# Optimization experiments

Measured on AMD Instinct MI355X. Metric: run time of the kernel, lower is better.

## Reference

```python
import jax, jax.numpy as jnp
import numpy as np

D = 1024        # n_embed
POS = 512       # n_pos_embed
H = 16          # heads
HS = D // H     # head size
DFF = 4 * D     # mlp hidden
EPS = 1e-5


def layernorm(x, g, b, eps=EPS):
    mu = jnp.mean(x, axis=-1, keepdims=True)
    var = jnp.var(x, axis=-1, keepdims=True)
    return (x - mu) * jax.lax.rsqrt(var + eps) * g + b


def setup_inputs() -> dict:
    key = jax.random.key(0)
    ks = jax.random.split(key, 12)
    std = 0.02
    inp = {
        "grid": jax.random.normal(ks[0], (8, 24, 24, D), dtype=jnp.float32),
        "query_pos": jax.random.normal(ks[1], (8, 1024, POS), dtype=jnp.float32),
        "Wq": jax.random.normal(ks[2], (POS, D), dtype=jnp.float32) * std,
        "Wk": jax.random.normal(ks[3], (D, D), dtype=jnp.float32) * std,
        "Wv": jax.random.normal(ks[4], (D, D), dtype=jnp.float32) * std,
        "Wo": jax.random.normal(ks[5], (D, D), dtype=jnp.float32) * std,
        "ln_grid_g": jnp.ones((D,), jnp.float32),
        "ln_grid_b": jnp.zeros((D,), jnp.float32),
        "ln_q_g": jnp.ones((POS,), jnp.float32),
        "ln_q_b": jnp.zeros((POS,), jnp.float32),
        "ln_mlp_g": jnp.ones((D,), jnp.float32),
        "ln_mlp_b": jnp.zeros((D,), jnp.float32),
        "W1": jax.random.normal(ks[6], (D, DFF), dtype=jnp.float32) * std,
        "b1": jnp.zeros((DFF,), jnp.float32),
        "W2": jax.random.normal(ks[7], (DFF, D), dtype=jnp.float32) * std,
        "b2": jnp.zeros((D,), jnp.float32),
    }
    return inp


def reference(grid, query_pos, Wq, Wk, Wv, Wo, ln_grid_g, ln_grid_b,
              ln_q_g, ln_q_b, ln_mlp_g, ln_mlp_b, W1, b1, W2, b2):
    B, N, M, d = grid.shape
    T = N * M
    grid_flat = grid.reshape(B, T, d)
    grid_norm = layernorm(grid_flat, ln_grid_g, ln_grid_b)
    K = jnp.einsum('btd,de->bte', grid_norm, Wk)
    V = jnp.einsum('btd,de->bte', grid_norm, Wv)
    query_norm = layernorm(query_pos, ln_q_g, ln_q_b)
    Q = jnp.einsum('blp,pe->ble', query_norm, Wq)
    L = Q.shape[1]
    # split heads: (B, H, L, HS)
    Qh = Q.reshape(B, L, H, HS).transpose(0, 2, 1, 3)
    Kh = K.reshape(B, T, H, HS).transpose(0, 2, 1, 3)
    Vh = V.reshape(B, T, H, HS).transpose(0, 2, 1, 3)
    scale = 1.0 / np.sqrt(HS).astype(np.float32)
    scores = jnp.einsum('bhld,bhmd->bhlm', Qh, Kh) * scale
    probs = jax.nn.softmax(scores, axis=-1)
    attn = jnp.einsum('bhlm,bhmd->bhld', probs, Vh)
    attn = attn.transpose(0, 2, 1, 3).reshape(B, L, d)
    attn = jnp.einsum('bld,de->ble', attn, Wo)
    x = Q + attn  # Q_proj residual
    x_norm = layernorm(x, ln_mlp_g, ln_mlp_b)
    mlp = jax.nn.gelu(x_norm @ W1 + b1) @ W2 + b2
    return x + mlp
```

## Files before the change

### kernel.cpp

```cpp
#include <hip/hip_runtime.h>

typedef __bf16 bf16x8 __attribute__((ext_vector_type(8)));
typedef float  f32x4  __attribute__((ext_vector_type(4)));
typedef short  s16x8  __attribute__((ext_vector_type(8)));

__device__ __forceinline__ unsigned short f2b(float f) {
  unsigned int u = __float_as_uint(f);
  u += 0x7fffu + ((u >> 16) & 1u);
  return (unsigned short)(u >> 16);
}
__device__ __forceinline__ float b2f(unsigned short h) {
  return __uint_as_float(((unsigned int)h) << 16);
}

__device__ __forceinline__ void gload_lds16(const unsigned short* g, unsigned short* l) {
  __builtin_amdgcn_global_load_lds((const __attribute__((address_space(1))) void*)g,
                                   (__attribute__((address_space(3))) void*)l, 16, 0, 0);
}

__device__ __forceinline__ void bar() {
  __builtin_amdgcn_sched_barrier(0);
  asm volatile("" ::: "memory");
  __builtin_amdgcn_s_barrier();
  asm volatile("" ::: "memory");
  __builtin_amdgcn_sched_barrier(0);
}

#define WAIT_LGKM0 do { asm volatile("s_waitcnt lgkmcnt(0)" ::: "memory"); \
                        __builtin_amdgcn_sched_barrier(0); } while (0)

__global__ __launch_bounds__(256) void transpose_w(const float* __restrict__ in,
                                                   unsigned short* __restrict__ out,
                                                   int R, int C) {
  __shared__ float t[32][33];
  int c0 = blockIdx.x * 32, r0 = blockIdx.y * 32;
  int tx = threadIdx.x & 31, ty = threadIdx.x >> 5;
  for (int i = ty; i < 32; i += 8)
    t[i][tx] = in[(size_t)(r0 + i) * C + (c0 + tx)];
  __syncthreads();
  for (int i = ty; i < 32; i += 8)
    out[(size_t)(c0 + i) * R + (r0 + tx)] = f2b(t[tx][i]);
}

__global__ __launch_bounds__(256) void ln_kernel(const float* __restrict__ in,
                                                 const float* __restrict__ g,
                                                 const float* __restrict__ b,
                                                 unsigned short* __restrict__ out,
                                                 int cols) {
  int row = blockIdx.x;
  const float* x = in + (size_t)row * cols;
  float s = 0.f, s2 = 0.f;
  for (int c = threadIdx.x * 4; c < cols; c += 1024) {
    float4 v = *(const float4*)(x + c);
    s  += v.x + v.y + v.z + v.w;
    s2 += v.x * v.x + v.y * v.y + v.z * v.z + v.w * v.w;
  }
#pragma unroll
  for (int o = 32; o > 0; o >>= 1) { s += __shfl_down(s, o); s2 += __shfl_down(s2, o); }
  __shared__ float rs[4], rs2[4];
  int w = threadIdx.x >> 6;
  if ((threadIdx.x & 63) == 0) { rs[w] = s; rs2[w] = s2; }
  __syncthreads();
  s  = rs[0] + rs[1] + rs[2] + rs[3];
  s2 = rs2[0] + rs2[1] + rs2[2] + rs2[3];
  float inv  = 1.f / (float)cols;
  float mean = s * inv;
  float var  = s2 * inv - mean * mean;
  float rstd = rsqrtf(var + 1e-5f);
  unsigned short* outp = out + (size_t)row * cols;
  for (int c = threadIdx.x * 4; c < cols; c += 1024) {
    float4 v = *(const float4*)(x + c);
    ushort4 ov;
    ov.x = f2b((v.x - mean) * rstd * g[c + 0] + b[c + 0]);
    ov.y = f2b((v.y - mean) * rstd * g[c + 1] + b[c + 1]);
    ov.z = f2b((v.z - mean) * rstd * g[c + 2] + b[c + 2]);
    ov.w = f2b((v.w - mean) * rstd * g[c + 3] + b[c + 3]);
    *(ushort4*)(outp + c) = ov;
  }
}

template <int BM, int BIAS, int GELU, int RES, int OUTBF>
__device__ __forceinline__ void gemm_body(const unsigned short* __restrict__ A,
                                          const unsigned short* __restrict__ Bt,
                                          float* __restrict__ Cf,
                                          unsigned short* __restrict__ Cb,
                                          const float* __restrict__ bias,
                                          const float* __restrict__ resf,
                                          const unsigned short* __restrict__ resb,
                                          int N, int K, int m0, int n0,
                                          unsigned short* L) {
  constexpr int MF = BM / 32;
  constexpr int MH = MF / 2;
  constexpr int LA = BM / 128;
  constexpr int LSTEP = (BM + 256) * 64;
  const int tid = threadIdx.x;
  const int w = tid >> 6, l = tid & 63;
  const int rl = l & 15, kb = l >> 4;
  const int wm = w >> 2, wn = w & 3;
  const int NT = K >> 6;
  const int colsw = ((l & 7) ^ (l >> 3)) * 8;
  const int lrow = l >> 3;

  auto stage = [&](int t, int half) {
    if (t >= NT) return;
    unsigned short* base = L + (t & 1) * LSTEP;
    if (half < 2) {
      const unsigned short* g = Bt + (size_t)(n0 + half * 128) * K + t * 64;
#pragma unroll
      for (int j = 0; j < 2; ++j) {
        int row = w * 16 + j * 8;
        gload_lds16(g + (size_t)(row + lrow) * K + colsw,
                    base + BM * 64 + half * 8192 + row * 64);
      }
    } else {
      const int h = half - 2;
      const unsigned short* g = A + (size_t)(m0 + h * (BM / 2)) * K + t * 64;
#pragma unroll
      for (int j = 0; j < LA; ++j) {
        int row = w * (8 * LA) + j * 8;
        gload_lds16(g + (size_t)(row + lrow) * K + colsw,
                    base + h * (BM / 2) * 64 + row * 64);
      }
    }
  };

  f32x4 acc[MF][4];
  f32x4 zz = {0.f, 0.f, 0.f, 0.f};
#pragma unroll
  for (int i = 0; i < MF; ++i)
#pragma unroll
    for (int j = 0; j < 4; ++j) acc[i][j] = zz;

  stage(0, 0); stage(0, 1); stage(0, 2); stage(0, 3);
  stage(1, 0); stage(1, 1); stage(1, 2);

  const int aoff = wm * (BM / 2) * 64;
  const int boff = BM * 64 + (wn >> 1) * 8192 + (wn & 1) * 64 * 64;

  for (int t = 0; t < NT; ++t) {
    const unsigned short* Lb = L + (t & 1) * LSTEP;
    if (t + 1 < NT) {
      if constexpr (LA == 2) asm volatile("s_waitcnt vmcnt(6)" ::: "memory");
      else                   asm volatile("s_waitcnt vmcnt(5)" ::: "memory");
    } else {
      asm volatile("s_waitcnt vmcnt(0)" ::: "memory");
    }
    __builtin_amdgcn_sched_barrier(0);
    bar();

    bf16x8 af[MH][2], bf[4][2];
#pragma unroll
    for (int mf = 0; mf < MH; ++mf)
#pragma unroll
      for (int kf = 0; kf < 2; ++kf)
        af[mf][kf] = *(const bf16x8*)(Lb + aoff + (mf * 16 + rl) * 64 +
                                      (((kf * 4 + kb) ^ (rl & 7)) * 8));
#pragma unroll
    for (int nf = 0; nf < 4; ++nf)
#pragma unroll
      for (int kf = 0; kf < 2; ++kf)
        bf[nf][kf] = *(const bf16x8*)(Lb + boff + (nf * 16 + rl) * 64 +
                                      (((kf * 4 + kb) ^ (rl & 7)) * 8));
    stage(t + 1, 3);
    WAIT_LGKM0;
    __builtin_amdgcn_s_setprio(1);
#pragma unroll
    for (int mf = 0; mf < MH; ++mf)
#pragma unroll
      for (int nf = 0; nf < 2; ++nf)
#pragma unroll
        for (int kf = 0; kf < 2; ++kf)
          acc[mf][nf] = __builtin_amdgcn_mfma_f32_16x16x32_bf16(af[mf][kf], bf[nf][kf], acc[mf][nf], 0, 0, 0);
    __builtin_amdgcn_s_setprio(0);
    bar();

    stage(t + 2, 0);
    __builtin_amdgcn_s_setprio(1);
#pragma unroll
    for (int mf = 0; mf < MH; ++mf)
#pragma unroll
      for (int nf = 2; nf < 4; ++nf)
#pragma unroll
        for (int kf = 0; kf < 2; ++kf)
          acc[mf][nf] = __builtin_amdgcn_mfma_f32_16x16x32_bf16(af[mf][kf], bf[nf][kf], acc[mf][nf], 0, 0, 0);
    __builtin_amdgcn_s_setprio(0);
    bar();

#pragma unroll
    for (int mf = 0; mf < MH; ++mf)
#pragma unroll
      for (int kf = 0; kf < 2; ++kf)
        af[mf][kf] = *(const bf16x8*)(Lb + aoff + ((MH + mf) * 16 + rl) * 64 +
                                      (((kf * 4 + kb) ^ (rl & 7)) * 8));
    stage(t + 2, 1);
    WAIT_LGKM0;
    __builtin_amdgcn_s_setprio(1);
#pragma unroll
    for (int mf = 0; mf < MH; ++mf)
#pragma unroll
      for (int nf = 0; nf < 2; ++nf)
#pragma unroll
        for (int kf = 0; kf < 2; ++kf)
          acc[MH + mf][nf] = __builtin_amdgcn_mfma_f32_16x16x32_bf16(af[mf][kf], bf[nf][kf], acc[MH + mf][nf], 0, 0, 0);
    __builtin_amdgcn_s_setprio(0);
    bar();

    stage(t + 2, 2);
    __builtin_amdgcn_s_setprio(1);
#pragma unroll
    for (int mf = 0; mf < MH; ++mf)
#pragma unroll
      for (int nf = 2; nf < 4; ++nf)
#pragma unroll
        for (int kf = 0; kf < 2; ++kf)
          acc[MH + mf][nf] = __builtin_amdgcn_mfma_f32_16x16x32_bf16(af[mf][kf], bf[nf][kf], acc[MH + mf][nf], 0, 0, 0);
    __builtin_amdgcn_s_setprio(0);
  }

  bar();

  float bias_v[4];
  if (BIAS) {
#pragma unroll
    for (int nf = 0; nf < 4; ++nf) bias_v[nf] = bias[n0 + wn * 64 + nf * 16 + rl];
  }
  unsigned short* patch  = L + w * (16 * 72);
  float*          patchf = ((float*)L) + w * (16 * 72);

#pragma unroll
  for (int mf = 0; mf < MF; ++mf) {
#pragma unroll
    for (int nf = 0; nf < 4; ++nf) {
#pragma unroll
      for (int r = 0; r < 4; ++r) {
        float v = acc[mf][nf][r];
        if (BIAS) v += bias_v[nf];
        if (GELU) {
          float t2 = 1.5957691f * (v + 0.044715f * v * v * v);
          float e = __expf(fminf(t2, 60.f));
          v = v * e / (e + 1.f);
        }
        int prow = kb * 4 + r, pcol = nf * 16 + rl;
        if (OUTBF) patch[prow * 72 + pcol] = f2b(v);
        else       patchf[prow * 72 + pcol] = v;
      }
    }
    WAIT_LGKM0;
    if (OUTBF) {
#pragma unroll
      for (int half = 0; half < 2; ++half) {
        int prow = half * 8 + (l >> 3);
        int pcol = (l & 7) * 8;
        s16x8 vv = *(const s16x8*)(patch + prow * 72 + pcol);
        int grow = m0 + wm * (BM / 2) + mf * 16 + prow;
        int gcol = n0 + wn * 64 + pcol;
        *(s16x8*)(Cb + (size_t)grow * N + gcol) = vv;
      }
    } else {
#pragma unroll
      for (int p = 0; p < 4; ++p) {
        int prow = p * 4 + (l >> 4);
        int pcol = (l & 15) * 4;
        float4 vv = *(const float4*)(patchf + prow * 72 + pcol);
        int grow = m0 + wm * (BM / 2) + mf * 16 + prow;
        int gcol = n0 + wn * 64 + pcol;
        if (RES == 1) {
          float4 rv = *(const float4*)(resf + (size_t)grow * N + gcol);
          vv.x += rv.x; vv.y += rv.y; vv.z += rv.z; vv.w += rv.w;
        }
        if (RES == 2) {
          ushort4 rv = *(const ushort4*)(resb + (size_t)grow * N + gcol);
          vv.x += b2f(rv.x); vv.y += b2f(rv.y); vv.z += b2f(rv.z); vv.w += b2f(rv.w);
        }
        *(float4*)(Cf + (size_t)grow * N + gcol) = vv;
      }
    }
    WAIT_LGKM0;
  }
}

template <int BM, int BIAS, int GELU, int RES, int OUTBF>
__global__ __launch_bounds__(512) void gemm256(const unsigned short* __restrict__ A,
                                               const unsigned short* __restrict__ Bt,
                                               float* __restrict__ Cf,
                                               unsigned short* __restrict__ Cb,
                                               const float* __restrict__ bias,
                                               const float* __restrict__ resf,
                                               const unsigned short* __restrict__ resb,
                                               int N, int K) {
  __shared__ unsigned short L[2 * (BM + 256) * 64];
  gemm_body<BM, BIAS, GELU, RES, OUTBF>(A, Bt, Cf, Cb, bias, resf, resb, N, K,
                                        blockIdx.x * BM, blockIdx.y * 256, L);
}

__global__ __launch_bounds__(512) void kvq_gemm(const unsigned short* __restrict__ gn,
                                                const unsigned short* __restrict__ Wkt,
                                                unsigned short* __restrict__ Kb,
                                                const unsigned short* __restrict__ Wvt,
                                                unsigned short* __restrict__ Vt2,
                                                const unsigned short* __restrict__ qn,
                                                const unsigned short* __restrict__ Wqt,
                                                unsigned short* __restrict__ Qbf) {
  __shared__ unsigned short L[2 * (128 + 256) * 64];
  const int x = blockIdx.x;
  if (x < 144) {
    gemm_body<128, 0, 0, 0, 1>(gn, Wkt, nullptr, Kb, nullptr, nullptr, nullptr,
                               1024, 1024, (x % 36) * 128, (x / 36) * 256, L);
  } else if (x < 288) {
    const int x2 = x - 144;
    gemm_body<128, 0, 0, 0, 1>(Wvt, gn, nullptr, Vt2, nullptr, nullptr, nullptr,
                               4608, 1024, (x2 % 8) * 128, (x2 / 8) * 256, L);
  } else {
    const int x3 = x - 288;
    gemm_body<128, 0, 0, 0, 1>(qn, Wqt, nullptr, Qbf, nullptr, nullptr, nullptr,
                               1024, 512, (x3 % 64) * 128, (x3 / 64) * 256, L);
  }
}

__global__ __launch_bounds__(256) void attn_mfma(const unsigned short* __restrict__ Qb,
                                                 const unsigned short* __restrict__ Kb,
                                                 const unsigned short* __restrict__ Vtb,
                                                 unsigned short* __restrict__ Ob) {
  __shared__ unsigned short Qs[64 * 64];
  __shared__ unsigned short Ks[2][64 * 64];
  __shared__ unsigned short Vs[2][64 * 64];
  __shared__ unsigned short PsT[4][16 * 64];

  const int t = threadIdx.x, w = t >> 6, l = t & 63;
  const int b = blockIdx.z, h = blockIdx.y, q0 = blockIdx.x * 64;
  const int rl = l & 15, kb = l >> 4;

  auto stage64 = [&](unsigned short* lds, const unsigned short* g, int gstride) {
#pragma unroll
    for (int p = 0; p < 2; ++p) {
      int row = p * 32 + w * 8 + (l >> 3);
      const unsigned short* src = g + (size_t)row * gstride + (((l & 7) ^ (row & 7)) * 8);
      gload_lds16(src, lds + p * 2048 + w * 512);
    }
  };

  const unsigned short* Qg = Qb + ((size_t)(b * 1024 + q0) * 1024 + h * 64);
  auto Kg = [&](int kt) { return Kb + ((size_t)(b * 576 + kt * 64) * 1024 + h * 64); };
  auto Vg = [&](int kt) { return Vtb + ((size_t)(h * 64) * 4608 + b * 576 + kt * 64); };

  stage64(Qs, Qg, 1024);
  stage64(Ks[0], Kg(0), 1024);
  stage64(Vs[0], Vg(0), 4608);
  __syncthreads();

  bf16x8 qf[2];
  {
    int row = w * 16 + rl;
#pragma unroll
    for (int kf = 0; kf < 2; ++kf)
      qf[kf] = *(const bf16x8*)(Qs + row * 64 + (((kf * 4 + kb) ^ (row & 7)) * 8));
  }

  float m_run = -1e30f, l_run = 0.f;
  f32x4 accOT[4];
  f32x4 zz = {0.f, 0.f, 0.f, 0.f};
#pragma unroll
  for (int df = 0; df < 4; ++df) accOT[df] = zz;

  unsigned short* pw = &PsT[w][0];

  for (int kt = 0; kt < 9; ++kt) {
    const int buf = kt & 1;
    if (kt + 1 < 9) {
      stage64(Ks[buf ^ 1], Kg(kt + 1), 1024);
      stage64(Vs[buf ^ 1], Vg(kt + 1), 4608);
    }

    f32x4 accS[4];
#pragma unroll
    for (int nf = 0; nf < 4; ++nf) accS[nf] = zz;
#pragma unroll
    for (int nf = 0; nf < 4; ++nf) {
      int row = nf * 16 + rl;
#pragma unroll
      for (int kf = 0; kf < 2; ++kf) {
        bf16x8 kfrag = *(const bf16x8*)(Ks[buf] + row * 64 + (((kf * 4 + kb) ^ (row & 7)) * 8));
        accS[nf] = __builtin_amdgcn_mfma_f32_16x16x32_bf16(kfrag, qf[kf], accS[nf], 0, 0, 0);
      }
    }

    float sv[4][4];
#pragma unroll
    for (int nf = 0; nf < 4; ++nf)
#pragma unroll
      for (int r = 0; r < 4; ++r) sv[nf][r] = accS[nf][r] * 0.125f;

    float rm = -1e30f;
#pragma unroll
    for (int nf = 0; nf < 4; ++nf)
#pragma unroll
      for (int r = 0; r < 4; ++r) rm = fmaxf(rm, sv[nf][r]);
    rm = fmaxf(rm, __shfl_xor(rm, 16));
    rm = fmaxf(rm, __shfl_xor(rm, 32));
    float mn = fmaxf(m_run, rm);
    float al = __expf(m_run - mn);
    m_run = mn;
    float rs = 0.f;
#pragma unroll
    for (int nf = 0; nf < 4; ++nf)
#pragma unroll
      for (int r = 0; r < 4; ++r) {
        sv[nf][r] = __expf(sv[nf][r] - mn);
        rs += sv[nf][r];
      }
    rs += __shfl_xor(rs, 16);
    rs += __shfl_xor(rs, 32);
    l_run = l_run * al + rs;

#pragma unroll
    for (int nf = 0; nf < 4; ++nf)
#pragma unroll
      for (int r = 0; r < 4; ++r) {
        int k = nf * 16 + kb * 4 + r;
        pw[rl * 64 + (((k >> 3) ^ (rl & 7)) * 8) + (k & 7)] = f2b(sv[nf][r]);
      }

#pragma unroll
    for (int df = 0; df < 4; ++df)
#pragma unroll
      for (int r = 0; r < 4; ++r) accOT[df][r] *= al;

    WAIT_LGKM0;

    bf16x8 pf[2];
#pragma unroll
    for (int ks = 0; ks < 2; ++ks)
      pf[ks] = *(const bf16x8*)(pw + rl * 64 + (((ks * 4 + kb) ^ (rl & 7)) * 8));
#pragma unroll
    for (int df = 0; df < 4; ++df) {
      int row = df * 16 + rl;
#pragma unroll
      for (int ks = 0; ks < 2; ++ks) {
        bf16x8 vfrag = *(const bf16x8*)(Vs[buf] + row * 64 + (((ks * 4 + kb) ^ (row & 7)) * 8));
        accOT[df] = __builtin_amdgcn_mfma_f32_16x16x32_bf16(vfrag, pf[ks], accOT[df], 0, 0, 0);
      }
    }

    __syncthreads();
  }

  float linv = 1.f / l_run;
#pragma unroll
  for (int df = 0; df < 4; ++df) {
    ushort4 ov;
    ov.x = f2b(accOT[df][0] * linv);
    ov.y = f2b(accOT[df][1] * linv);
    ov.z = f2b(accOT[df][2] * linv);
    ov.w = f2b(accOT[df][3] * linv);
    size_t qg = (size_t)(b * 1024 + q0 + w * 16 + rl);
    *(ushort4*)(Ob + qg * 1024 + h * 64 + df * 16 + kb * 4) = ov;
  }
}

extern "C" void kernel_launch(void* const* d_in, const int* in_sizes, int n_in,
                              void* d_out, int out_size, void* d_ws, size_t ws_size,
                              hipStream_t stream) {
  const float* grid_in = (const float*)d_in[0];
  const float* qpos    = (const float*)d_in[1];
  const float* Wq      = (const float*)d_in[2];
  const float* Wk      = (const float*)d_in[3];
  const float* Wv      = (const float*)d_in[4];
  const float* Wo      = (const float*)d_in[5];
  const float* g_grid  = (const float*)d_in[6];
  const float* b_grid  = (const float*)d_in[7];
  const float* g_q     = (const float*)d_in[8];
  const float* b_q     = (const float*)d_in[9];
  const float* g_mlp   = (const float*)d_in[10];
  const float* b_mlp   = (const float*)d_in[11];
  const float* W1      = (const float*)d_in[12];
  const float* b1      = (const float*)d_in[13];
  const float* W2      = (const float*)d_in[14];
  const float* b2      = (const float*)d_in[15];

  char* ws = (char*)d_ws;
  size_t off = 0;
  auto alloc = [&](size_t bytes) -> void* {
    void* p = ws + off;
    off = (off + bytes + 255) & ~(size_t)255;
    return p;
  };

  unsigned short* Wqt = (unsigned short*)alloc((size_t)1024 * 512 * 2);
  unsigned short* Wkt = (unsigned short*)alloc((size_t)1024 * 1024 * 2);
  unsigned short* Wvt = (unsigned short*)alloc((size_t)1024 * 1024 * 2);
  unsigned short* Wot = (unsigned short*)alloc((size_t)1024 * 1024 * 2);
  unsigned short* W1t = (unsigned short*)alloc((size_t)4096 * 1024 * 2);
  unsigned short* W2t = (unsigned short*)alloc((size_t)1024 * 4096 * 2);
  unsigned short* gn  = (unsigned short*)alloc((size_t)4608 * 1024 * 2);
  unsigned short* qn  = (unsigned short*)alloc((size_t)8192 * 512 * 2);
  unsigned short* Kb  = (unsigned short*)alloc((size_t)4608 * 1024 * 2);
  unsigned short* Qbf = (unsigned short*)alloc((size_t)8192 * 1024 * 2);
  unsigned short* atb = (unsigned short*)alloc((size_t)8192 * 1024 * 2);
  float*          xf  = (float*)alloc((size_t)8192 * 1024 * 4);
  unsigned short* xnb = (unsigned short*)alloc((size_t)8192 * 1024 * 2);
  unsigned short* hb  = (unsigned short*)alloc((size_t)8192 * 4096 * 2);
  unsigned short* Vt2 = hb;
  (void)ws_size; (void)in_sizes; (void)n_in; (void)out_size;

  transpose_w<<<dim3(32, 16), 256, 0, stream>>>(Wq, Wqt, 512, 1024);
  transpose_w<<<dim3(32, 32), 256, 0, stream>>>(Wk, Wkt, 1024, 1024);
  transpose_w<<<dim3(32, 32), 256, 0, stream>>>(Wv, Wvt, 1024, 1024);
  transpose_w<<<dim3(32, 32), 256, 0, stream>>>(Wo, Wot, 1024, 1024);
  transpose_w<<<dim3(128, 32), 256, 0, stream>>>(W1, W1t, 1024, 4096);
  transpose_w<<<dim3(32, 128), 256, 0, stream>>>(W2, W2t, 4096, 1024);

  ln_kernel<<<4608, 256, 0, stream>>>(grid_in, g_grid, b_grid, gn, 1024);
  ln_kernel<<<8192, 256, 0, stream>>>(qpos, g_q, b_q, qn, 512);

  kvq_gemm<<<544, 512, 0, stream>>>(gn, Wkt, Kb, Wvt, Vt2, qn, Wqt, Qbf);

  attn_mfma<<<dim3(16, 16, 8), 256, 0, stream>>>(Qbf, Kb, Vt2, atb);

  gemm256<128, 0, 0, 2, 0><<<dim3(64, 4), 512, 0, stream>>>(atb, Wot, xf, nullptr, nullptr, nullptr, Qbf, 1024, 1024);

  ln_kernel<<<8192, 256, 0, stream>>>(xf, g_mlp, b_mlp, xnb, 1024);
  gemm256<256, 1, 1, 0, 1><<<dim3(32, 16), 512, 0, stream>>>(xnb, W1t, nullptr, hb, b1, nullptr, nullptr, 4096, 1024);
  gemm256<128, 1, 0, 1, 0><<<dim3(64, 4), 512, 0, stream>>>(hb, W2t, (float*)d_out, nullptr, b2, xf, nullptr, 1024, 4096);
}
```

Measured before the change: 351.5 us.

## Fuse weight transposes and input layernorms into one prep kernel; enlarge KVQ GEMM tiles

Merges the six weight transpose launches and two layernorm launches into a single prep kernel that dispatches on block index, to cut launch overhead and per-kernel tail gaps. The fused K/V/Q projection GEMM switches from 128-row to 256-row tiles, halving the block count so more data is reused per tile. The larger tile doubles the shared-memory footprint and leaves about one wave of blocks across the CUs, which can cost occupancy and load balance.

```diff
diff --git a/kernel.cpp b/kernel.cpp
--- a/kernel.cpp
+++ b/kernel.cpp
@@ -29,11 +29,11 @@
 #define WAIT_LGKM0 do { asm volatile("s_waitcnt lgkmcnt(0)" ::: "memory"); \
                         __builtin_amdgcn_sched_barrier(0); } while (0)
 
-__global__ __launch_bounds__(256) void transpose_w(const float* __restrict__ in,
-                                                   unsigned short* __restrict__ out,
-                                                   int R, int C) {
+__device__ __forceinline__ void tw_body(const float* __restrict__ in,
+                                        unsigned short* __restrict__ out,
+                                        int R, int C, int bx, int by) {
   __shared__ float t[32][33];
-  int c0 = blockIdx.x * 32, r0 = blockIdx.y * 32;
+  int c0 = bx * 32, r0 = by * 32;
   int tx = threadIdx.x & 31, ty = threadIdx.x >> 5;
   for (int i = ty; i < 32; i += 8)
     t[i][tx] = in[(size_t)(r0 + i) * C + (c0 + tx)];
@@ -42,12 +42,11 @@
     out[(size_t)(c0 + i) * R + (r0 + tx)] = f2b(t[tx][i]);
 }
 
-__global__ __launch_bounds__(256) void ln_kernel(const float* __restrict__ in,
-                                                 const float* __restrict__ g,
-                                                 const float* __restrict__ b,
-                                                 unsigned short* __restrict__ out,
-                                                 int cols) {
-  int row = blockIdx.x;
+__device__ __forceinline__ void ln_body(const float* __restrict__ in,
+                                        const float* __restrict__ g,
+                                        const float* __restrict__ b,
+                                        unsigned short* __restrict__ out,
+                                        int cols, int row) {
   const float* x = in + (size_t)row * cols;
   float s = 0.f, s2 = 0.f;
   for (int c = threadIdx.x * 4; c < cols; c += 1024) {
@@ -77,6 +76,43 @@
     ov.w = f2b((v.w - mean) * rstd * g[c + 3] + b[c + 3]);
     *(ushort4*)(outp + c) = ov;
   }
+}
+
+__global__ __launch_bounds__(256) void prep_kernel(
+    const float* __restrict__ grid_in, const float* __restrict__ g_grid,
+    const float* __restrict__ b_grid, unsigned short* __restrict__ gn,
+    const float* __restrict__ qpos, const float* __restrict__ g_q,
+    const float* __restrict__ b_q, unsigned short* __restrict__ qn,
+    const float* __restrict__ Wq, unsigned short* __restrict__ Wqt,
+    const float* __restrict__ Wk, unsigned short* __restrict__ Wkt,
+    const float* __restrict__ Wv, unsigned short* __restrict__ Wvt,
+    const float* __restrict__ Wo, unsigned short* __restrict__ Wot,
+    const float* __restrict__ W1, unsigned short* __restrict__ W1t,
+    const float* __restrict__ W2, unsigned short* __restrict__ W2t) {
+  int x = blockIdx.x;
+  if (x < 4608) { ln_body(grid_in, g_grid, b_grid, gn, 1024, x); return; }
+  x -= 4608;
+  if (x < 8192) { ln_body(qpos, g_q, b_q, qn, 512, x); return; }
+  x -= 8192;
+  if (x < 512)  { tw_body(Wq, Wqt, 512, 1024, x % 32, x / 32); return; }
+  x -= 512;
+  if (x < 1024) { tw_body(Wk, Wkt, 1024, 1024, x % 32, x / 32); return; }
+  x -= 1024;
+  if (x < 1024) { tw_body(Wv, Wvt, 1024, 1024, x % 32, x / 32); return; }
+  x -= 1024;
+  if (x < 1024) { tw_body(Wo, Wot, 1024, 1024, x % 32, x / 32); return; }
+  x -= 1024;
+  if (x < 4096) { tw_body(W1, W1t, 1024, 4096, x % 128, x / 128); return; }
+  x -= 4096;
+  tw_body(W2, W2t, 4096, 1024, x % 32, x / 32);
+}
+
+__global__ __launch_bounds__(256) void ln_kernel(const float* __restrict__ in,
+                                                 const float* __restrict__ g,
+                                                 const float* __restrict__ b,
+                                                 unsigned short* __restrict__ out,
+                                                 int cols) {
+  ln_body(in, g, b, out, cols, blockIdx.x);
 }
 
 template <int BM, int BIAS, int GELU, int RES, int OUTBF>
@@ -301,19 +337,19 @@
                                                 const unsigned short* __restrict__ qn,
                                                 const unsigned short* __restrict__ Wqt,
                                                 unsigned short* __restrict__ Qbf) {
-  __shared__ unsigned short L[2 * (128 + 256) * 64];
+  __shared__ unsigned short L[2 * (256 + 256) * 64];
   const int x = blockIdx.x;
-  if (x < 144) {
-    gemm_body<128, 0, 0, 0, 1>(gn, Wkt, nullptr, Kb, nullptr, nullptr, nullptr,
-                               1024, 1024, (x % 36) * 128, (x / 36) * 256, L);
-  } else if (x < 288) {
-    const int x2 = x - 144;
-    gemm_body<128, 0, 0, 0, 1>(Wvt, gn, nullptr, Vt2, nullptr, nullptr, nullptr,
-                               4608, 1024, (x2 % 8) * 128, (x2 / 8) * 256, L);
+  if (x < 72) {
+    gemm_body<256, 0, 0, 0, 1>(gn, Wkt, nullptr, Kb, nullptr, nullptr, nullptr,
+                               1024, 1024, (x % 18) * 256, (x / 18) * 256, L);
+  } else if (x < 144) {
+    const int x2 = x - 72;
+    gemm_body<256, 0, 0, 0, 1>(Wvt, gn, nullptr, Vt2, nullptr, nullptr, nullptr,
+                               4608, 1024, (x2 % 4) * 256, (x2 / 4) * 256, L);
   } else {
-    const int x3 = x - 288;
-    gemm_body<128, 0, 0, 0, 1>(qn, Wqt, nullptr, Qbf, nullptr, nullptr, nullptr,
-                               1024, 512, (x3 % 64) * 128, (x3 / 64) * 256, L);
+    const int x3 = x - 144;
+    gemm_body<256, 0, 0, 0, 1>(qn, Wqt, nullptr, Qbf, nullptr, nullptr, nullptr,
+                               1024, 512, (x3 % 32) * 256, (x3 / 32) * 256, L);
   }
 }
 
@@ -502,17 +538,12 @@
   unsigned short* Vt2 = hb;
   (void)ws_size; (void)in_sizes; (void)n_in; (void)out_size;
 
-  transpose_w<<<dim3(32, 16), 256, 0, stream>>>(Wq, Wqt, 512, 1024);
-  transpose_w<<<dim3(32, 32), 256, 0, stream>>>(Wk, Wkt, 1024, 1024);
-  transpose_w<<<dim3(32, 32), 256, 0, stream>>>(Wv, Wvt, 1024, 1024);
-  transpose_w<<<dim3(32, 32), 256, 0, stream>>>(Wo, Wot, 1024, 1024);
-  transpose_w<<<dim3(128, 32), 256, 0, stream>>>(W1, W1t, 1024, 4096);
-  transpose_w<<<dim3(32, 128), 256, 0, stream>>>(W2, W2t, 4096, 1024);
-
-  ln_kernel<<<4608, 256, 0, stream>>>(grid_in, g_grid, b_grid, gn, 1024);
-  ln_kernel<<<8192, 256, 0, stream>>>(qpos, g_q, b_q, qn, 512);
-
-  kvq_gemm<<<544, 512, 0, stream>>>(gn, Wkt, Kb, Wvt, Vt2, qn, Wqt, Qbf);
+  prep_kernel<<<24576, 256, 0, stream>>>(grid_in, g_grid, b_grid, gn,
+                                         qpos, g_q, b_q, qn,
+                                         Wq, Wqt, Wk, Wkt, Wv, Wvt,
+                                         Wo, Wot, W1, W1t, W2, W2t);
+
+  kvq_gemm<<<272, 512, 0, stream>>>(gn, Wkt, Kb, Wvt, Vt2, qn, Wqt, Qbf);
 
   attn_mfma<<<dim3(16, 16, 8), 256, 0, stream>>>(Qbf, Kb, Vt2, atb);
 
```

Result: faster. 312.6 us (-11.1%).
